# Performance work log

Hardware: AMD Instinct MI355X
Metric: run time of the kernel (lower is better)

Reference implementation:

```python
import jax, jax.numpy as jnp
import numpy as np

SENS = 200
DM = 128
NMAPS = 2
NLAYERS = 2
TH = 0.01
EPS = 1e-5
BATCH = 8
SEQ = 96
HEADS = 8


def setup_inputs() -> dict:
    key = jax.random.key(0)
    ks = jax.random.split(key, 8)
    x = jax.random.normal(ks[0], (BATCH, SENS, SEQ, DM), jnp.float32)
    attn_s = jax.random.uniform(ks[1], (1, BATCH, HEADS, SENS, SENS), jnp.float32)
    supports = jax.random.uniform(ks[2], (SENS, SENS), jnp.float32)
    W_conv = jax.random.normal(ks[3], (NMAPS, NLAYERS, DM, DM), jnp.float32) * 0.05
    b_conv = jnp.zeros((NMAPS, NLAYERS, DM), jnp.float32)
    bn_gamma = jnp.ones((NMAPS, DM), jnp.float32)
    bn_beta = jnp.zeros((NMAPS, DM), jnp.float32)
    W_out = jax.random.normal(ks[4], (NMAPS * DM, DM), jnp.float32) * 0.05
    b_out = jnp.zeros((DM,), jnp.float32)
    return dict(x=x, attn_s=attn_s, supports=supports, W_conv=W_conv,
                b_conv=b_conv, bn_gamma=bn_gamma, bn_beta=bn_beta,
                W_out=W_out, b_out=b_out)


def _process_map(A):
    # make_symmetric: lower triangle + mirrored strict lower triangle
    A = jnp.tril(A) + jnp.tril(A, -1).T
    # clamp: threshold on absolute value; note original returns |A| thresholded
    Aa = jnp.abs(A)
    A = jnp.where(Aa > TH, Aa, jnp.zeros_like(Aa))
    # SparseTensor.from_dense(A).t()
    return A.T


def _gcn_norm(adj_t):
    # GCNConv default: add self-loops (weight 1), symmetric D^-1/2 A D^-1/2
    A = adj_t + jnp.eye(adj_t.shape[0], dtype=adj_t.dtype)
    deg = A.sum(axis=1)
    d = jnp.where(deg > 0, jax.lax.rsqrt(deg), jnp.zeros_like(deg))
    return d[:, None] * A * d[None, :]


def reference(x, attn_s, supports, W_conv, b_conv, bn_gamma, bn_beta, W_out, b_out):
    B, N, S, D = x.shape
    # reshape_mat: [B,N,S,D] -> [B*S, N, D]
    xr = x.transpose(0, 2, 1, 3).reshape(B * S, N, D)

    # supports: [data map, adaptive map from attention (mean over batch, heads)]
    maps = [_process_map(supports), _process_map(attn_s[0].mean(axis=(0, 1)))]

    gcn_outputs = []
    for i in range(NMAPS):
        An = _gcn_norm(maps[i])  # [N,N]
        h = jnp.zeros_like(xr[..., :1]) * 0.0  # placeholder replaced below
        h = None
        for l in range(NLAYERS):
            xw = jnp.einsum('bnf,fg->bng', xr, W_conv[i, l])
            hl = jnp.einsum('mn,bng->bmg', An, xw) + b_conv[i, l]
            h = hl if h is None else h + hl
        # BatchNorm1d over feature channel (training-mode batch stats, biased var)
        mu = h.mean(axis=(0, 1))
        var = h.var(axis=(0, 1))
        hn = (h - mu) * jax.lax.rsqrt(var + EPS) * bn_gamma[i] + bn_beta[i]
        gcn_outputs.append(jax.nn.relu(hn))

    cat = jnp.concatenate(gcn_outputs, axis=-1)  # [B*S, N, NMAPS*DM]
    y = jax.nn.relu(jnp.einsum('bnc,cd->bnd', cat, W_out) + b_out)
    # inverse_reshape_mat: [B*S, N, D] -> [B, N, S, D]
    return y.reshape(B, S, N, D).transpose(0, 2, 1, 3)
```

## Files before the change

### kernel.cpp

```cpp
#include <hip/hip_runtime.h>

#define SENS 200
#define DM 128
#define SEQ 96
#define NB 8
#define BS 768
#define NTOT 153600
#define TH 0.01f
#define BN_EPS 1e-5f
#define MPAD 224
#define KP 208
#define XWS 208
#define ASROW 68

typedef __attribute__((ext_vector_type(8)))  __bf16 bf16x8;
typedef __attribute__((ext_vector_type(4)))  __bf16 bf16x4;
typedef __attribute__((ext_vector_type(16))) float  f32x16;

__device__ __forceinline__ f32x16 mfma32(bf16x8 a, bf16x8 b, f32x16 c) {
    return __builtin_amdgcn_mfma_f32_32x32x16_bf16(a, b, c, 0, 0, 0);
}
__device__ __forceinline__ bf16x8 join8(bf16x4 a, bf16x4 b) {
    bf16x8 r;
    #pragma unroll
    for (int j = 0; j < 4; ++j) { r[j] = a[j]; r[j + 4] = b[j]; }
    return r;
}

__global__ void attn_mean_kernel(const float* __restrict__ attn, float* __restrict__ mapA) {
    int idx = blockIdx.x * 256 + threadIdx.x;
    if (idx >= SENS * SENS) return;
    float s = 0.f;
    #pragma unroll 8
    for (int q = 0; q < 64; ++q) s += attn[(size_t)q * SENS * SENS + idx];
    mapA[idx] = s * (1.0f / 64.0f);
}

__global__ void build_map_kernel(const float* __restrict__ supports, const float* __restrict__ mapA,
                                 float* __restrict__ M, float* __restrict__ deg) {
    __shared__ float red[256];
    int m = blockIdx.x, map = blockIdx.y, j = threadIdx.x;
    const float* src = (map == 0) ? supports : mapA;
    float v = 0.f;
    if (j < SENS) {
        float sym = (m >= j) ? src[m * SENS + j] : src[j * SENS + m];
        float a = fabsf(sym);
        v = (a > TH) ? a : 0.f;
        M[(size_t)map * SENS * SENS + m * SENS + j] = v;
    }
    red[j] = v;
    __syncthreads();
    for (int off = 128; off > 0; off >>= 1) {
        if (j < off) red[j] += red[j + off];
        __syncthreads();
    }
    if (j == 0) deg[map * SENS + m] = red[0] + 1.0f;
}

__global__ __launch_bounds__(256) void prep2_kernel(
    const float* __restrict__ M, const float* __restrict__ deg,
    const float* __restrict__ W_conv, const float* __restrict__ b_conv,
    const float* __restrict__ W_out,
    __bf16* __restrict__ Anb, __bf16* __restrict__ Wt, __bf16* __restrict__ Wot,
    float* __restrict__ bsum, float* __restrict__ bnacc)
{
    const int bid = blockIdx.x, t = threadIdx.x;
    if (bid < 2 * MPAD) {
        const int map = bid / MPAD, m = bid % MPAD;
        const int j = t;
        if (j < KP) {
            float val = 0.f;
            if (m < SENS && j < SENS) {
                float a = M[((size_t)map * SENS + m) * SENS + j] + ((m == j) ? 1.f : 0.f);
                val = rsqrtf(deg[map * SENS + m]) * a * rsqrtf(deg[map * SENS + j]);
            }
            Anb[(((size_t)map * 13 + (j >> 4)) * MPAD + m) * 16 + (j & 15)] = (__bf16)val;
        }
    } else {
        const int idx = (bid - 2 * MPAD) * 256 + t;
        if (idx < 32768) {
            const int map = idx >> 14, g = (idx >> 7) & 127, f = idx & 127;
            const float* wp = W_conv + (size_t)map * 2 * DM * DM + f * DM + g;
            Wt[(((size_t)map * 8 + (f >> 4)) * DM + g) * 16 + (f & 15)] = (__bf16)(wp[0] + wp[DM * DM]);
        } else if (idx < 65536) {
            const int k = idx - 32768, d = k >> 8, c = k & 255;
            Wot[(((size_t)(c >> 4)) * DM + d) * 16 + (c & 15)] = (__bf16)W_out[c * DM + d];
        } else if (idx < 65792) {
            const int k = idx - 65536, map = k >> 7, g = k & 127;
            bsum[k] = b_conv[(map * 2) * DM + g] + b_conv[(map * 2 + 1) * DM + g];
        } else if (idx < 66304) {
            bnacc[idx - 65792] = 0.f;
        }
    }
}

__global__ __launch_bounds__(896, 2) void conv_kernel(
    const float* __restrict__ x, const __bf16* __restrict__ Anb,
    const __bf16* __restrict__ Wt, const float* __restrict__ bsum,
    __bf16* __restrict__ h, float* __restrict__ bnacc)
{
    __shared__ __bf16 xw[128 * XWS];
    __shared__ float bnred[2 * 128 * 7];
    const int bs = blockIdx.x;
    const int b = bs / SEQ, s = bs % SEQ;
    const int t = threadIdx.x, w = t >> 6, lane = t & 63;
    const int l31 = lane & 31, hi = lane >> 5;
    const int strip = w >> 1, gh = w & 1;

    const int n = strip * 32 + l31;
    const bool valid = (n < SENS);
    const float* xrow = x + (((size_t)b * SENS + (valid ? n : 0)) * SEQ + s) * DM + hi * 8;

    #pragma unroll 1
    for (int map = 0; map < 2; ++map) {
        if (map) {
            __syncthreads();
            if (t < 256) {
                const int sq = t >> 7, g = t & 127;
                float ssum = 0.f;
                #pragma unroll
                for (int k = 0; k < 7; ++k) ssum += bnred[(sq * 128 + g) * 7 + k];
                atomicAdd(&bnacc[sq * 256 + g], ssum);
            }
        }
        {
            f32x16 acc[2];
            #pragma unroll
            for (int gt2 = 0; gt2 < 2; ++gt2)
                #pragma unroll
                for (int r = 0; r < 16; ++r) acc[gt2][r] = 0.f;
            const __bf16* wb = Wt + (((size_t)map * 8) * DM + gh * 64 + l31) * 16 + hi * 8;
            #pragma unroll
            for (int kc = 0; kc < 8; ++kc) {
                float4 v0 = *(const float4*)(xrow + kc * 16);
                float4 v1 = *(const float4*)(xrow + kc * 16 + 4);
                bf16x8 bfrag;
                bfrag[0] = (__bf16)v0.x; bfrag[1] = (__bf16)v0.y;
                bfrag[2] = (__bf16)v0.z; bfrag[3] = (__bf16)v0.w;
                bfrag[4] = (__bf16)v1.x; bfrag[5] = (__bf16)v1.y;
                bfrag[6] = (__bf16)v1.z; bfrag[7] = (__bf16)v1.w;
                if (!valid) {
                    #pragma unroll
                    for (int j = 0; j < 8; ++j) bfrag[j] = (__bf16)0.f;
                }
                const __bf16* wp = wb + (size_t)kc * DM * 16;
                acc[0] = mfma32(*(const bf16x8*)wp, bfrag, acc[0]);
                acc[1] = mfma32(*(const bf16x8*)(wp + 32 * 16), bfrag, acc[1]);
            }
            if (n < KP) {
                #pragma unroll
                for (int gt2 = 0; gt2 < 2; ++gt2)
                    #pragma unroll
                    for (int r = 0; r < 16; ++r) {
                        const int g = (gh * 2 + gt2) * 32 + (r & 3) + 8 * (r >> 2) + 4 * hi;
                        xw[g * XWS + n] = (__bf16)acc[gt2][r];
                    }
            }
        }
        __syncthreads();

        f32x16 acc2[2];
        #pragma unroll
        for (int gt2 = 0; gt2 < 2; ++gt2)
            #pragma unroll
            for (int r = 0; r < 16; ++r) acc2[gt2][r] = 0.f;
        {
            const __bf16* ab = Anb + (((size_t)map * 13) * MPAD + strip * 32 + l31) * 16 + hi * 8;
            #pragma unroll 2
            for (int kc = 0; kc < 13; ++kc) {
                bf16x8 afrag = *(const bf16x8*)(ab + (size_t)kc * MPAD * 16);
                #pragma unroll
                for (int gt2 = 0; gt2 < 2; ++gt2) {
                    bf16x8 bfrag = *(const bf16x8*)(xw + ((gh * 2 + gt2) * 32 + l31) * XWS + kc * 16 + hi * 8);
                    acc2[gt2] = mfma32(afrag, bfrag, acc2[gt2]);
                }
            }
        }
        #pragma unroll
        for (int gt2 = 0; gt2 < 2; ++gt2) {
            const int gt = gh * 2 + gt2;
            const float bias = bsum[map * DM + gt * 32 + l31];
            bf16x8 h0, h1;
            float s2 = 0.f, q = 0.f;
            #pragma unroll
            for (int r = 0; r < 16; ++r) {
                const float v = acc2[gt2][r] + bias;
                if (r < 8) h0[r] = (__bf16)v; else h1[r - 8] = (__bf16)v;
                const int m = strip * 32 + (r & 3) + 8 * (r >> 2) + 4 * hi;
                if (m < SENS) { s2 += v; q += v * v; }
            }
            __bf16* hp = h + ((((size_t)(bs * 2 + map) * 7 + strip) * 4 + gt) * 64 + lane) * 16;
            *(bf16x8*)hp = h0;
            *(bf16x8*)(hp + 8) = h1;
            s2 += __shfl_xor(s2, 32);
            q += __shfl_xor(q, 32);
            if (hi == 0) {
                bnred[((0 * 128) + gt * 32 + l31) * 7 + strip] = s2;
                bnred[((1 * 128) + gt * 32 + l31) * 7 + strip] = q;
            }
        }
    }
    __syncthreads();
    if (t < 256) {
        const int sq = t >> 7, g = t & 127;
        float ssum = 0.f;
        #pragma unroll
        for (int k = 0; k < 7; ++k) ssum += bnred[(sq * 128 + g) * 7 + k];
        atomicAdd(&bnacc[sq * 256 + DM + g], ssum);
    }
}

__device__ __forceinline__ void out_stage(int cn, int t, int bs,
                                          const __bf16* __restrict__ h,
                                          const float* sc_s, const float* sh_s,
                                          __bf16* dst)
{
    const int mapn = cn >> 1;
    const __bf16* hb = h + ((size_t)(bs * 2 + mapn) * 28 + (cn & 1) * 2) * 1024;
    #pragma unroll
    for (int hf = 0; hf < 2; ++hf) {
        bf16x8 vv[2];
        #pragma unroll
        for (int it = 0; it < 2; ++it) {
            const int idx = (hf * 2 + it) * 512 + t;
            if (idx < 1792)
                vv[it] = *(const bf16x8*)(hb + ((size_t)(idx >> 8) * 4 + ((idx >> 7) & 1)) * 1024
                                              + ((idx >> 1) & 63) * 16 + (idx & 1) * 8);
        }
        #pragma unroll
        for (int it = 0; it < 2; ++it) {
            const int idx = (hf * 2 + it) * 512 + t;
            if (idx < 1792) {
                const int half = idx & 1, lane_s = (idx >> 1) & 63;
                const int ctl = (idx >> 7) & 1, strip = idx >> 8;
                const int cl = ctl * 32 + (lane_s & 31);
                const int cg = mapn * DM + (cn & 1) * 64 + cl;
                const float scv = sc_s[cg], shv = sh_s[cg];
                const int mbase = strip * 32 + 4 * (lane_s >> 5) + 16 * half;
                #pragma unroll
                for (int q2 = 0; q2 < 8; ++q2) {
                    const int row = mbase + (q2 & 3) + 8 * (q2 >> 2);
                    const float fv = (float)vv[it][q2] * scv + shv;
                    dst[row * ASROW + cl] = (__bf16)fmaxf(fv, 0.f);
                }
            }
        }
    }
}

__global__ __launch_bounds__(512) void out_kernel(
    const __bf16* __restrict__ h, const __bf16* __restrict__ Wot,
    const float* __restrict__ bnacc,
    const float* __restrict__ gamma, const float* __restrict__ beta,
    const float* __restrict__ b_out, float* __restrict__ out)
{
    __shared__ __bf16 As[MPAD * ASROW];
    __shared__ float sc_s[256], sh_s[256];
    const int bs = blockIdx.x;
    const int b = bs / SEQ, s = bs % SEQ;
    const int t = threadIdx.x, w = t >> 6, lane = t & 63;
    const int l31 = lane & 31, hi = lane >> 5;
    const int dct = w & 3, sbase = w >> 2;
    if (t < 256) {
        const float mu = bnacc[t] * (1.f / (float)NTOT);
        const float var = bnacc[256 + t] * (1.f / (float)NTOT) - mu * mu;
        const float sc = gamma[t] * rsqrtf(var + BN_EPS);
        sc_s[t] = sc;
        sh_s[t] = beta[t] - mu * sc;
    }
    f32x16 acc[4];
    {
        const float bo = b_out[dct * 32 + l31];
        #pragma unroll
        for (int i = 0; i < 4; ++i)
            #pragma unroll
            for (int r = 0; r < 16; ++r) acc[i][r] = bo;
    }
    __syncthreads();
    for (int c = 0; c < 4; ++c) {
        out_stage(c, t, bs, h, sc_s, sh_s, &As[0]);
        __syncthreads();
        #pragma unroll
        for (int kc = 0; kc < 4; ++kc) {
            bf16x8 bfrag = *(const bf16x8*)(Wot + ((size_t)(c * 4 + kc) * DM + dct * 32 + l31) * 16 + hi * 8);
            #pragma unroll
            for (int i = 0; i < 4; ++i) {
                const int strip = sbase + 2 * i;
                if (strip >= 7) break;
                const __bf16* ap = &As[(strip * 32 + l31) * ASROW + kc * 16 + hi * 8];
                acc[i] = mfma32(join8(*(const bf16x4*)ap, *(const bf16x4*)(ap + 4)), bfrag, acc[i]);
            }
        }
        if (c < 3) __syncthreads();
    }
    #pragma unroll
    for (int i = 0; i < 4; ++i) {
        const int strip = sbase + 2 * i;
        if (strip >= 7) break;
        #pragma unroll
        for (int r = 0; r < 16; ++r) {
            const int m = strip * 32 + (r & 3) + 8 * (r >> 2) + 4 * hi;
            if (m < SENS)
                out[(((size_t)b * SENS + m) * SEQ + s) * DM + dct * 32 + l31] = fmaxf(acc[i][r], 0.f);
        }
    }
}

extern "C" void kernel_launch(void* const* d_in, const int* in_sizes, int n_in,
                              void* d_out, int out_size, void* d_ws, size_t ws_size,
                              hipStream_t stream) {
    const float* x        = (const float*)d_in[0];
    const float* attn     = (const float*)d_in[1];
    const float* supports = (const float*)d_in[2];
    const float* W_conv   = (const float*)d_in[3];
    const float* b_conv   = (const float*)d_in[4];
    const float* gamma    = (const float*)d_in[5];
    const float* beta     = (const float*)d_in[6];
    const float* W_out    = (const float*)d_in[7];
    const float* b_out    = (const float*)d_in[8];
    float* out = (float*)d_out;
    char* base = (char*)d_ws;

    float*  mapA  = (float*)(base + 0);
    float*  Mbuf  = (float*)(base + 160000);
    float*  deg   = (float*)(base + 480000);
    float*  bnacc = (float*)(base + 481664);
    float*  bsum  = (float*)(base + 483712);
    __bf16* Wt    = (__bf16*)(base + 484736);
    __bf16* Wot   = (__bf16*)(base + 550272);
    __bf16* Anb   = (__bf16*)(base + 615808);
    __bf16* h     = (__bf16*)(base + 1048576);

    attn_mean_kernel<<<157, 256, 0, stream>>>(attn, mapA);
    build_map_kernel<<<dim3(SENS, 2), 256, 0, stream>>>(supports, mapA, Mbuf, deg);
    prep2_kernel<<<2 * MPAD + 260, 256, 0, stream>>>(Mbuf, deg, W_conv, b_conv, W_out,
                                                     Anb, Wt, Wot, bsum, bnacc);
    conv_kernel<<<BS, 896, 0, stream>>>(x, Anb, Wt, bsum, h, bnacc);
    out_kernel<<<BS, 512, 0, stream>>>(h, Wot, bnacc, gamma, beta, b_out, out);
}
```

Baseline: 252.8 us.

## Split fused conv kernel into separate XW GEMM and graph-conv kernels via global buffer

Replaces the single fused conv kernel, which computed X·W into shared memory and then A·XW per block, with two kernels. The first writes bf16 XW fragments to a global workspace in MFMA-ready layout, using permlane32 swaps to repack outputs. The second reads them back to do the adjacency GEMM, bias and BN statistics. This lowers shared memory use and block size, but adds a round trip through global memory of about 80MB. Falls back to the old fused kernel when the workspace is too small.

After: 279.3 us. 10.5% more time.

```diff
diff --git a/kernel.cpp b/kernel.cpp
--- a/kernel.cpp
+++ b/kernel.cpp
@@ -12,6 +12,7 @@
 #define KP 208
 #define XWS 208
 #define ASROW 68
+#define XW_ELEMS_PER_MAP 20447232ull
 
 typedef __attribute__((ext_vector_type(8)))  __bf16 bf16x8;
 typedef __attribute__((ext_vector_type(4)))  __bf16 bf16x4;
@@ -25,6 +26,19 @@
     #pragma unroll
     for (int j = 0; j < 4; ++j) { r[j] = a[j]; r[j + 4] = b[j]; }
     return r;
+}
+__device__ __forceinline__ unsigned pk2(float a, float b) {
+    union { unsigned u; __bf16 hh[2]; } t;
+    t.hh[0] = (__bf16)a; t.hh[1] = (__bf16)b;
+    return t.u;
+}
+__device__ __forceinline__ void permswap(unsigned &a, unsigned &b) {
+    asm("v_permlane32_swap_b32 %0, %1" : "+v"(a), "+v"(b));
+}
+__device__ __forceinline__ bf16x8 frag4(unsigned a, unsigned b, unsigned c, unsigned d) {
+    union { unsigned u[4]; bf16x8 v; } t;
+    t.u[0] = a; t.u[1] = b; t.u[2] = c; t.u[3] = d;
+    return t.v;
 }
 
 __global__ void attn_mean_kernel(const float* __restrict__ attn, float* __restrict__ mapA) {
@@ -91,6 +105,127 @@
         } else if (idx < 66304) {
             bnacc[idx - 65792] = 0.f;
         }
+    }
+}
+
+__global__ __launch_bounds__(448) void xw_kernel(
+    const float* __restrict__ x, const __bf16* __restrict__ Wt,
+    __bf16* __restrict__ xwg, int map0, int nmaps)
+{
+    const int bs = blockIdx.x;
+    const int b = bs / SEQ, s = bs % SEQ;
+    const int t = threadIdx.x, w = t >> 6, lane = t & 63;
+    const int l31 = lane & 31, hi = lane >> 5;
+    const int n = w * 32 + l31;
+    const bool valid = (n < SENS);
+    const float* xrow = x + (((size_t)b * SENS + (valid ? n : 0)) * SEQ + s) * DM + hi * 8;
+
+    bf16x8 xf[8];
+    #pragma unroll
+    for (int kc = 0; kc < 8; ++kc) {
+        float4 v0 = *(const float4*)(xrow + kc * 16);
+        float4 v1 = *(const float4*)(xrow + kc * 16 + 4);
+        bf16x8 f;
+        f[0] = (__bf16)v0.x; f[1] = (__bf16)v0.y; f[2] = (__bf16)v0.z; f[3] = (__bf16)v0.w;
+        f[4] = (__bf16)v1.x; f[5] = (__bf16)v1.y; f[6] = (__bf16)v1.z; f[7] = (__bf16)v1.w;
+        if (!valid) {
+            #pragma unroll
+            for (int j = 0; j < 8; ++j) f[j] = (__bf16)0.f;
+        }
+        xf[kc] = f;
+    }
+
+    for (int mi = 0; mi < nmaps; ++mi) {
+        const int map = map0 + mi;
+        __bf16* xwm = xwg + (size_t)mi * XW_ELEMS_PER_MAP;
+        #pragma unroll
+        for (int gt = 0; gt < 4; ++gt) {
+            f32x16 acc;
+            #pragma unroll
+            for (int r = 0; r < 16; ++r) acc[r] = 0.f;
+            const __bf16* wb = Wt + (((size_t)map * 8) * DM + gt * 32 + l31) * 16 + hi * 8;
+            #pragma unroll
+            for (int kc = 0; kc < 8; ++kc)
+                acc = mfma32(xf[kc], *(const bf16x8*)(wb + (size_t)kc * DM * 16), acc);
+            {
+                unsigned w0 = pk2(acc[0], acc[1]),  w1 = pk2(acc[2], acc[3]);
+                unsigned w2 = pk2(acc[4], acc[5]),  w3 = pk2(acc[6], acc[7]);
+                permswap(w0, w2); permswap(w1, w3);
+                *(bf16x8*)(xwm + (((size_t)bs * 13 + 2 * w) * 128 + gt * 32 + l31) * 16 + hi * 8)
+                    = frag4(w0, w1, w2, w3);
+            }
+            if (w < 6) {
+                unsigned w0 = pk2(acc[8], acc[9]),   w1 = pk2(acc[10], acc[11]);
+                unsigned w2 = pk2(acc[12], acc[13]), w3 = pk2(acc[14], acc[15]);
+                permswap(w0, w2); permswap(w1, w3);
+                *(bf16x8*)(xwm + (((size_t)bs * 13 + 2 * w + 1) * 128 + gt * 32 + l31) * 16 + hi * 8)
+                    = frag4(w0, w1, w2, w3);
+            }
+        }
+    }
+}
+
+__global__ __launch_bounds__(448) void gc_kernel(
+    const __bf16* __restrict__ Anb, const __bf16* __restrict__ xwg,
+    const float* __restrict__ bsum, __bf16* __restrict__ h,
+    float* __restrict__ bnacc, int map0, int nmaps)
+{
+    __shared__ float bnred[2][2 * 128 * 7];
+    const int bs = blockIdx.x;
+    const int t = threadIdx.x, w = t >> 6, lane = t & 63;
+    const int l31 = lane & 31, hi = lane >> 5;
+
+    for (int mi = 0; mi < nmaps; ++mi) {
+        const int map = map0 + mi;
+        const __bf16* xwm = xwg + (size_t)mi * XW_ELEMS_PER_MAP;
+        f32x16 acc2[4];
+        #pragma unroll
+        for (int gt = 0; gt < 4; ++gt)
+            #pragma unroll
+            for (int r = 0; r < 16; ++r) acc2[gt][r] = 0.f;
+        {
+            const __bf16* ab = Anb + (((size_t)map * 13) * MPAD + w * 32 + l31) * 16 + hi * 8;
+            const __bf16* xb = xwm + ((size_t)bs * 13 * 128 + l31) * 16 + hi * 8;
+            #pragma unroll 2
+            for (int kc = 0; kc < 13; ++kc) {
+                bf16x8 afrag = *(const bf16x8*)(ab + (size_t)kc * MPAD * 16);
+                #pragma unroll
+                for (int gt = 0; gt < 4; ++gt) {
+                    bf16x8 bfrag = *(const bf16x8*)(xb + ((size_t)kc * 128 + gt * 32) * 16);
+                    acc2[gt] = mfma32(afrag, bfrag, acc2[gt]);
+                }
+            }
+        }
+        #pragma unroll
+        for (int gt = 0; gt < 4; ++gt) {
+            const float bias = bsum[map * DM + gt * 32 + l31];
+            bf16x8 h0, h1;
+            float s2 = 0.f, q = 0.f;
+            #pragma unroll
+            for (int r = 0; r < 16; ++r) {
+                const float v = acc2[gt][r] + bias;
+                if (r < 8) h0[r] = (__bf16)v; else h1[r - 8] = (__bf16)v;
+                const int m = w * 32 + (r & 3) + 8 * (r >> 2) + 4 * hi;
+                if (m < SENS) { s2 += v; q += v * v; }
+            }
+            __bf16* hp = h + ((((size_t)(bs * 2 + map) * 7 + w) * 4 + gt) * 64 + lane) * 16;
+            *(bf16x8*)hp = h0;
+            *(bf16x8*)(hp + 8) = h1;
+            s2 += __shfl_xor(s2, 32);
+            q += __shfl_xor(q, 32);
+            if (hi == 0) {
+                bnred[mi][((0 * 128) + gt * 32 + l31) * 7 + w] = s2;
+                bnred[mi][((1 * 128) + gt * 32 + l31) * 7 + w] = q;
+            }
+        }
+    }
+    __syncthreads();
+    for (int i = t; i < nmaps * 256; i += 448) {
+        const int mi = i >> 8, sq = (i >> 7) & 1, g = i & 127;
+        float ssum = 0.f;
+        #pragma unroll
+        for (int k = 0; k < 7; ++k) ssum += bnred[mi][(sq * 128 + g) * 7 + k];
+        atomicAdd(&bnacc[sq * 256 + (map0 + mi) * DM + g], ssum);
     }
 }
 
@@ -330,11 +465,26 @@
     __bf16* Wot   = (__bf16*)(base + 550272);
     __bf16* Anb   = (__bf16*)(base + 615808);
     __bf16* h     = (__bf16*)(base + 1048576);
+    __bf16* xwg   = (__bf16*)(base + 89128960);
+
+    const size_t XW_BYTES_PER_MAP = XW_ELEMS_PER_MAP * 2;
+    const size_t need_both  = 89128960ull + 2 * XW_BYTES_PER_MAP;
+    const size_t need_split = 89128960ull + 1 * XW_BYTES_PER_MAP;
 
     attn_mean_kernel<<<157, 256, 0, stream>>>(attn, mapA);
     build_map_kernel<<<dim3(SENS, 2), 256, 0, stream>>>(supports, mapA, Mbuf, deg);
     prep2_kernel<<<2 * MPAD + 260, 256, 0, stream>>>(Mbuf, deg, W_conv, b_conv, W_out,
                                                      Anb, Wt, Wot, bsum, bnacc);
-    conv_kernel<<<BS, 896, 0, stream>>>(x, Anb, Wt, bsum, h, bnacc);
+    if (ws_size >= need_both) {
+        xw_kernel<<<BS, 448, 0, stream>>>(x, Wt, xwg, 0, 2);
+        gc_kernel<<<BS, 448, 0, stream>>>(Anb, xwg, bsum, h, bnacc, 0, 2);
+    } else if (ws_size >= need_split) {
+        for (int m = 0; m < 2; ++m) {
+            xw_kernel<<<BS, 448, 0, stream>>>(x, Wt, xwg, m, 1);
+            gc_kernel<<<BS, 448, 0, stream>>>(Anb, xwg, bsum, h, bnacc, m, 1);
+        }
+    } else {
+        conv_kernel<<<BS, 896, 0, stream>>>(x, Anb, Wt, bsum, h, bnacc);
+    }
     out_kernel<<<BS, 512, 0, stream>>>(h, Wot, bnacc, gamma, beta, b_out, out);
 }
```
